# Optimization experiments

Hardware: AMD Instinct MI355X
Metric: run time of the kernel (lower is better)

The kernel has to match this reference:

```python
import jax, jax.numpy as jnp
import numpy as np

N, CS, CZ, CH, H, PQK, PV = 768, 384, 128, 16, 12, 4, 8
INF, EPS = 1e5, 1e-8


def setup_inputs() -> dict:
    key = jax.random.key(0)
    ks = jax.random.split(key, 12)
    w = lambda k, i, o: (jax.random.normal(k, (i, o), jnp.float32) * 0.02)
    inp = {
        's': jax.random.normal(ks[0], (N, CS), jnp.float32),
        'z': jax.random.normal(ks[1], (N, N, CZ), jnp.float32),
        'rot': jax.random.normal(ks[2], (N, 3, 3), jnp.float32),
        'trans': jax.random.normal(ks[3], (N, 3), jnp.float32),
        'mask': jnp.ones((N,), jnp.float32),
        'W_q': w(ks[4], CS, H * CH), 'b_q': jnp.zeros((H * CH,), jnp.float32),
        'W_kv': w(ks[5], CS, 2 * H * CH), 'b_kv': jnp.zeros((2 * H * CH,), jnp.float32),
        'W_qp': w(ks[6], CS, H * PQK * 3), 'b_qp': jnp.zeros((H * PQK * 3,), jnp.float32),
        'W_kvp': w(ks[7], CS, H * (PQK + PV) * 3), 'b_kvp': jnp.zeros((H * (PQK + PV) * 3,), jnp.float32),
        'W_b': w(ks[8], CZ, H), 'b_b': jnp.zeros((H,), jnp.float32),
        'head_weights': jnp.full((H,), 0.541324854612918, jnp.float32),  # softplus^-1(1)
        'W_out': w(ks[9], H * (CZ + CH + PV * 4), CS), 'b_out': jnp.zeros((CS,), jnp.float32),
    }
    return inp


def reference(s, z, rot, trans, mask, W_q, b_q, W_kv, b_kv, W_qp, b_qp, W_kvp, b_kvp,
              W_b, b_b, head_weights, W_out, b_out):
    n = s.shape[0]
    # scalar q/k/v
    q = (s @ W_q + b_q).reshape(n, H, CH)
    kv = (s @ W_kv + b_kv).reshape(n, H, 2 * CH)
    k, v = kv[..., :CH], kv[..., CH:]

    def make_points(W, b, P):
        p = (s @ W + b).reshape(n, 3, H * P)         # 3 contiguous coord chunks (x,y,z)
        p = jnp.transpose(p, (0, 2, 1))              # [n, H*P, 3]
        p = jnp.einsum('nij,npj->npi', rot, p) + trans[:, None, :]  # global frame
        return p.reshape(n, H, P, 3)

    q_pts = make_points(W_qp, b_qp, PQK)
    kv_pts = make_points(W_kvp, b_kvp, PQK + PV)
    k_pts, v_pts = kv_pts[:, :, :PQK], kv_pts[:, :, PQK:]

    b_pair = z @ W_b + b_b                                       # [n, n, H]
    a = jnp.einsum('qhc,khc->hqk', q, k) * np.sqrt(1.0 / (3 * CH))
    a = a + np.sqrt(1.0 / 3) * jnp.transpose(b_pair, (2, 0, 1))

    # point-distance attention term
    d2 = jnp.sum((q_pts[:, None] - k_pts[None]) ** 2, axis=-1)   # [q, k, H, Pqk]
    hw = jax.nn.softplus(head_weights) * np.sqrt(1.0 / (3 * (PQK * 9.0 / 2)))
    pt_att = -0.5 * jnp.sum(d2 * hw[None, None, :, None], axis=-1)  # [q, k, H]
    a = a + jnp.transpose(pt_att, (2, 0, 1))

    sq_mask = INF * (mask[:, None] * mask[None, :] - 1.0)
    a = jax.nn.softmax(a + sq_mask[None], axis=-1)               # [H, q, k]

    o = jnp.einsum('hqk,khc->qhc', a, v).reshape(n, H * CH)
    o_pt = jnp.einsum('hqk,khpc->qhpc', a, v_pts)                # [q, H, Pv, 3]
    o_pt = jnp.einsum('nba,nhpb->nhpa', rot, o_pt - trans[:, None, None, :])  # invert_apply
    o_pt_norm = jnp.sqrt(jnp.sum(o_pt ** 2, axis=-1) + EPS).reshape(n, H * PV)
    o_pt_flat = o_pt.reshape(n, H * PV, 3)
    o_pair = jnp.einsum('hqk,qkc->qhc', a, z).reshape(n, H * CZ)

    cat = jnp.concatenate([o, o_pt_flat[..., 0], o_pt_flat[..., 1], o_pt_flat[..., 2],
                           o_pt_norm, o_pair], axis=-1)          # [n, H*(CZ+CH+Pv*4)]
    return cat @ W_out + b_out
```

## Files before the change

### kernel.cpp

```cpp
#include <hip/hip_runtime.h>
#include <hip/hip_bf16.h>
#include <math.h>

#define NRES 768
#define CS   384
#define CZ   128
#define CH   16
#define NH   12
#define PQK  4
#define PV   8
#define QCOLS   (NH*CH)
#define KVCOLS  (2*NH*CH)
#define QPCOLS  (NH*PQK*3)
#define KVPCOLS (NH*(PQK+PV)*3)
#define CATC    (NH*(CZ+CH+PV*4))
#define NN      (NRES*NRES)

__global__ __launch_bounds__(256) void proj_kernel(
    const float* __restrict__ s,
    const float* __restrict__ Wq,  const float* __restrict__ bq,
    const float* __restrict__ Wkv, const float* __restrict__ bkv,
    const float* __restrict__ Wqp, const float* __restrict__ bqp,
    const float* __restrict__ Wkvp,const float* __restrict__ bkvp,
    float* __restrict__ proj_q, float* __restrict__ proj_kv,
    float* __restrict__ proj_qp, float* __restrict__ proj_kvp)
{
    __shared__ float Al[32][68];
    __shared__ float Bl[32][52];
    const int mt = blockIdx.x;
    const int gc0 = blockIdx.y * 48;
    const float* W; const float* bb; int ncol; float* dst; int c0;
    if (gc0 < 192)      { W=Wq;   bb=bq;   ncol=QCOLS;   dst=proj_q;   c0=gc0; }
    else if (gc0 < 576) { W=Wkv;  bb=bkv;  ncol=KVCOLS;  dst=proj_kv;  c0=gc0-192; }
    else if (gc0 < 720) { W=Wqp;  bb=bqp;  ncol=QPCOLS;  dst=proj_qp;  c0=gc0-576; }
    else                { W=Wkvp; bb=bkvp; ncol=KVPCOLS; dst=proj_kvp; c0=gc0-720; }
    const int tid = threadIdx.x;
    const int m0 = (tid & 15)*4;
    const int n0 = (tid >> 4)*3;
    float acc[4][3] = {};
    for (int kc = 0; kc < CS; kc += 32) {
        #pragma unroll
        for (int f = tid; f < 512; f += 256) {
            int r = f >> 3, c4 = (f & 7)*4;
            float4 v = *(const float4*)(s + (size_t)(mt*64+r)*CS + kc + c4);
            Al[c4][r]=v.x; Al[c4+1][r]=v.y; Al[c4+2][r]=v.z; Al[c4+3][r]=v.w;
        }
        for (int f = tid; f < 384; f += 256) {
            int r = f / 12, c4 = (f % 12)*4;
            *(float4*)&Bl[r][c4] = *(const float4*)(W + (size_t)(kc+r)*ncol + c0 + c4);
        }
        __syncthreads();
        #pragma unroll
        for (int kk = 0; kk < 32; ++kk) {
            float4 a = *(const float4*)&Al[kk][m0];
            float b0 = Bl[kk][n0], b1 = Bl[kk][n0+1], b2 = Bl[kk][n0+2];
            acc[0][0]+=a.x*b0; acc[0][1]+=a.x*b1; acc[0][2]+=a.x*b2;
            acc[1][0]+=a.y*b0; acc[1][1]+=a.y*b1; acc[1][2]+=a.y*b2;
            acc[2][0]+=a.z*b0; acc[2][1]+=a.z*b1; acc[2][2]+=a.z*b2;
            acc[3][0]+=a.w*b0; acc[3][1]+=a.w*b1; acc[3][2]+=a.w*b2;
        }
        __syncthreads();
    }
    #pragma unroll
    for (int r = 0; r < 4; ++r)
        #pragma unroll
        for (int c = 0; c < 3; ++c)
            dst[(size_t)(mt*64+m0+r)*ncol + c0+n0+c] = acc[r][c] + bb[c0+n0+c];
}

__global__ __launch_bounds__(256) void rotpts_kernel(
    const float* __restrict__ rot, const float* __restrict__ trans,
    const float* __restrict__ proj_q, const float* __restrict__ proj_kv,
    const float* __restrict__ proj_qp, const float* __restrict__ proj_kvp,
    const float* __restrict__ b_out,
    float* __restrict__ qfrag, float* __restrict__ kcat, float* __restrict__ vcatT,
    float* __restrict__ out)
{
    int g = blockIdx.x*256 + threadIdx.x;
    const int S0 = NRES*48;
    const int S1 = S0 + NRES*432;
    const int S2 = S1 + NRES*192;
    const int S3 = S2 + NRES*384;
    const int S4 = S3 + NRES*CS;
    if (g < S0) {
        int n = g/48, rem = g%48;
        int h = rem>>2, p = rem&3;
        float p0 = proj_qp[(size_t)n*QPCOLS + rem];
        float p1 = proj_qp[(size_t)n*QPCOLS + 48 + rem];
        float p2 = proj_qp[(size_t)n*QPCOLS + 96 + rem];
        const float* Rm = rot + (size_t)n*9; const float* t = trans + (size_t)n*3;
        float* dq = qfrag + ((size_t)n*12 + h)*28 + 16 + p*3;
        #pragma unroll
        for (int i = 0; i < 3; ++i)
            dq[i] = Rm[i*3]*p0 + Rm[i*3+1]*p1 + Rm[i*3+2]*p2 + t[i];
    } else if (g < S1) {
        int g2 = g - S0;
        int n = g2 % 768, t = g2 / 768;
        int h = t/36, u = t%36, p = u/3, i = u%3;
        int col = h*12 + p;
        float p0 = proj_kvp[(size_t)n*KVPCOLS + col];
        float p1 = proj_kvp[(size_t)n*KVPCOLS + 144 + col];
        float p2 = proj_kvp[(size_t)n*KVPCOLS + 288 + col];
        float val = rot[(size_t)n*9 + i*3]*p0 + rot[(size_t)n*9 + i*3+1]*p1
                  + rot[(size_t)n*9 + i*3+2]*p2 + trans[(size_t)n*3 + i];
        if (p < PQK) kcat[(size_t)(h*28 + 16 + p*3 + i)*NRES + n] = val;
        else         vcatT[(size_t)(h*40 + 16 + (p-4)*3 + i)*NRES + n] = val;
    } else if (g < S2) {
        int g3 = g - S1;
        int n = g3 / 192, c = g3 % 192;
        int h = c >> 4, cc = c & 15;
        qfrag[((size_t)n*12 + h)*28 + cc] = proj_q[(size_t)n*QCOLS + c];
    } else if (g < S3) {
        int g4 = g - S2;
        int n = g4 % 768, col = g4 / 768;
        int h = col >> 5, cc = col & 31;
        float val = proj_kv[(size_t)n*KVCOLS + col];
        if (cc < 16) kcat[(size_t)(h*28 + cc)*NRES + n] = val;
        else         vcatT[(size_t)(h*40 + (cc-16))*NRES + n] = val;
    } else if (g < S4) {
        int g5 = g - S3;
        out[g5] = b_out[g5 % CS];
    }
}

__global__ __launch_bounds__(256) void bias_kernel(
    const float* __restrict__ z, const float* __restrict__ mask,
    const float* __restrict__ W_b, const float* __restrict__ b_b,
    float* __restrict__ lg)
{
    int r = blockIdx.x*256 + threadIdx.x;
    int q = r / 768, k = r - q*768;
    const float4* zr = (const float4*)(z + (size_t)r*CZ);
    float acc[12] = {};
    #pragma unroll
    for (int c4 = 0; c4 < 32; ++c4) {
        float4 v = zr[c4];
        const float* w0 = W_b + c4*48;
        #pragma unroll
        for (int h = 0; h < 12; ++h)
            acc[h] += v.x*w0[h] + v.y*w0[12+h] + v.z*w0[24+h] + v.w*w0[36+h];
    }
    float mterm = 100000.0f*(mask[q]*mask[k] - 1.0f);
    const float scale_b = 0.5773502691896258f;
    #pragma unroll
    for (int h = 0; h < 12; ++h)
        lg[(size_t)h*NN + r] = scale_b*(acc[h] + b_b[h]) + mterm;
}

__global__ __launch_bounds__(256) void softmax_fused_kernel(
    float* __restrict__ lg, const float* __restrict__ qfrag, const float* __restrict__ kcat,
    const float* __restrict__ head_w, const float* __restrict__ vcatT,
    float* __restrict__ cat, float* __restrict__ optt)
{
    const int h = blockIdx.x % 12;
    const int q = (blockIdx.x / 12)*4 + (threadIdx.x >> 6);
    const int ln = threadIdx.x & 63;
    const float scale_qk = 0.14433756729740643f;
    float x = head_w[h];
    float sp = (x > 20.f) ? x : log1pf(__expf(x));
    float coef = -0.5f * sp * 0.13608276348795434f;

    float qf[28];
    const float* qp = qfrag + ((size_t)q*12 + h)*28;
    #pragma unroll
    for (int c = 0; c < 28; ++c) qf[c] = qp[c];

    float* arow = lg + (size_t)h*NN + (size_t)q*NRES;
    const float* kb = kcat + (size_t)h*28*NRES;
    float4 a[3];
    #pragma unroll
    for (int i = 0; i < 3; ++i) {
        a[i] = *(const float4*)(arow + ln*4 + i*256);
        float4 d = {0.f,0.f,0.f,0.f}, p2 = {0.f,0.f,0.f,0.f};
        #pragma unroll
        for (int c = 0; c < 16; ++c) {
            float4 kv = *(const float4*)(kb + (size_t)c*NRES + ln*4 + i*256);
            d.x += qf[c]*kv.x; d.y += qf[c]*kv.y; d.z += qf[c]*kv.z; d.w += qf[c]*kv.w;
        }
        #pragma unroll
        for (int c = 16; c < 28; ++c) {
            float4 kv = *(const float4*)(kb + (size_t)c*NRES + ln*4 + i*256);
            float t0 = qf[c]-kv.x, t1 = qf[c]-kv.y, t2 = qf[c]-kv.z, t3 = qf[c]-kv.w;
            p2.x += t0*t0; p2.y += t1*t1; p2.z += t2*t2; p2.w += t3*t3;
        }
        a[i].x += scale_qk*d.x + coef*p2.x;
        a[i].y += scale_qk*d.y + coef*p2.y;
        a[i].z += scale_qk*d.z + coef*p2.z;
        a[i].w += scale_qk*d.w + coef*p2.w;
    }
    float m = -1e30f;
    #pragma unroll
    for (int i=0;i<3;++i) m = fmaxf(m, fmaxf(fmaxf(a[i].x,a[i].y),fmaxf(a[i].z,a[i].w)));
    #pragma unroll
    for (int o=32;o>0;o>>=1) m = fmaxf(m, __shfl_xor(m,o,64));
    float ssum = 0.f;
    #pragma unroll
    for (int i=0;i<3;++i) {
        a[i].x = __expf(a[i].x-m); a[i].y = __expf(a[i].y-m);
        a[i].z = __expf(a[i].z-m); a[i].w = __expf(a[i].w-m);
        ssum += a[i].x + a[i].y + a[i].z + a[i].w;
    }
    #pragma unroll
    for (int o=32;o>0;o>>=1) ssum += __shfl_xor(ssum,o,64);
    float inv = 1.f/ssum;
    #pragma unroll
    for (int i=0;i<3;++i) {
        a[i].x*=inv; a[i].y*=inv; a[i].z*=inv; a[i].w*=inv;
        *(float4*)(arow + ln*4 + i*256) = a[i];
    }
    for (int col = 0; col < 40; ++col) {
        const float* vrow = vcatT + (size_t)(h*40+col)*NRES;
        float p = 0.f;
        #pragma unroll
        for (int i=0;i<3;++i) {
            float4 v = *(const float4*)(vrow + ln*4 + i*256);
            p += a[i].x*v.x + a[i].y*v.y + a[i].z*v.z + a[i].w*v.w;
        }
        #pragma unroll
        for (int o=32;o>0;o>>=1) p += __shfl_xor(p,o,64);
        if (ln == 0) {
            if (col < 16) cat[(size_t)q*CATC + h*16 + col] = p;
            else          optt[(size_t)q*288 + h*24 + (col-16)] = p;
        }
    }
}

__global__ __launch_bounds__(192) void opair_kernel(
    const float* __restrict__ z, const float* __restrict__ lg,
    const float* __restrict__ rot, const float* __restrict__ trans,
    const float* __restrict__ optt, float* __restrict__ cat)
{
    __shared__ float4 abuf4[2304];
    float* abuf = (float*)abuf4;
    const int q = blockIdx.x, tid = threadIdx.x;
    float* crow = cat + (size_t)q*CATC;

    for (int f = tid; f < 2304; f += 192) {
        int hh = f / 192, k4 = f % 192;
        abuf4[hh*192 + k4] = *(const float4*)(lg + (size_t)hh*NN + (size_t)q*NRES + k4*4);
    }
    __syncthreads();
    if (tid < 96) {
        int hh = tid>>3, p = tid&7;
        float b0 = optt[(size_t)q*288 + hh*24+p*3+0] - trans[q*3+0];
        float b1 = optt[(size_t)q*288 + hh*24+p*3+1] - trans[q*3+1];
        float b2 = optt[(size_t)q*288 + hh*24+p*3+2] - trans[q*3+2];
        const float* Rm = rot + (size_t)q*9;
        float v0 = Rm[0]*b0 + Rm[3]*b1 + Rm[6]*b2;
        float v1 = Rm[1]*b0 + Rm[4]*b1 + Rm[7]*b2;
        float v2 = Rm[2]*b0 + Rm[5]*b1 + Rm[8]*b2;
        crow[192 + tid] = v0;
        crow[288 + tid] = v1;
        crow[384 + tid] = v2;
        crow[480 + tid] = sqrtf(v0*v0 + v1*v1 + v2*v2 + 1e-8f);
    }
    const int h = tid >> 4, c8 = (tid & 15)*8;
    const float* zq = z + (size_t)q*NRES*CZ + c8;
    const float* ah = abuf + h*768;
    float4 acc0 = {0.f,0.f,0.f,0.f}, acc1 = {0.f,0.f,0.f,0.f};
    #pragma unroll 4
    for (int k = 0; k < NRES; ++k) {
        float aw = ah[k];
        float4 z0 = *(const float4*)(zq + (size_t)k*CZ);
        float4 z1 = *(const float4*)(zq + (size_t)k*CZ + 4);
        acc0.x += aw*z0.x; acc0.y += aw*z0.y; acc0.z += aw*z0.z; acc0.w += aw*z0.w;
        acc1.x += aw*z1.x; acc1.y += aw*z1.y; acc1.z += aw*z1.z; acc1.w += aw*z1.w;
    }
    *(float4*)(crow + 576 + h*128 + c8)     = acc0;
    *(float4*)(crow + 576 + h*128 + c8 + 4) = acc1;
}

__global__ __launch_bounds__(256) void outgemm_kernel(
    const float* __restrict__ cat, const float* __restrict__ W_out,
    float* __restrict__ out)
{
    __shared__ float Al[32][68];
    __shared__ float Bl[32][68];
    const int mt = blockIdx.x;
    const int nt = blockIdx.y;
    const int kt = blockIdx.z;
    const int tid = threadIdx.x;
    const int m0 = (tid & 15)*4, n0 = (tid >> 4)*4;
    float acc[4][4] = {};
    for (int ki = 0; ki < 11; ++ki) {
        int kc = kt*352 + ki*32;
        #pragma unroll
        for (int f = tid; f < 512; f += 256) {
            int r = f >> 3, c4 = (f & 7)*4;
            float4 v = *(const float4*)(cat + (size_t)(mt*64+r)*CATC + kc + c4);
            Al[c4][r]=v.x; Al[c4+1][r]=v.y; Al[c4+2][r]=v.z; Al[c4+3][r]=v.w;
        }
        #pragma unroll
        for (int f = tid; f < 512; f += 256) {
            int r = f >> 4, c4 = (f & 15)*4;
            *(float4*)&Bl[r][c4] = *(const float4*)(W_out + (size_t)(kc+r)*CS + nt*64 + c4);
        }
        __syncthreads();
        #pragma unroll
        for (int kk = 0; kk < 32; ++kk) {
            float4 a = *(const float4*)&Al[kk][m0];
            float4 b = *(const float4*)&Bl[kk][n0];
            acc[0][0]+=a.x*b.x; acc[0][1]+=a.x*b.y; acc[0][2]+=a.x*b.z; acc[0][3]+=a.x*b.w;
            acc[1][0]+=a.y*b.x; acc[1][1]+=a.y*b.y; acc[1][2]+=a.y*b.z; acc[1][3]+=a.y*b.w;
            acc[2][0]+=a.z*b.x; acc[2][1]+=a.z*b.y; acc[2][2]+=a.z*b.z; acc[2][3]+=a.z*b.w;
            acc[3][0]+=a.w*b.x; acc[3][1]+=a.w*b.y; acc[3][2]+=a.w*b.z; acc[3][3]+=a.w*b.w;
        }
        __syncthreads();
    }
    #pragma unroll
    for (int r = 0; r < 4; ++r)
        #pragma unroll
        for (int c = 0; c < 4; ++c)
            atomicAdd(&out[(size_t)(mt*64+m0+r)*CS + nt*64+n0+c], acc[r][c]);
}

extern "C" void kernel_launch(void* const* d_in, const int* in_sizes, int n_in,
                              void* d_out, int out_size, void* d_ws, size_t ws_size,
                              hipStream_t stream) {
    const float* s      = (const float*)d_in[0];
    const float* z      = (const float*)d_in[1];
    const float* rot    = (const float*)d_in[2];
    const float* trans  = (const float*)d_in[3];
    const float* mask   = (const float*)d_in[4];
    const float* W_q    = (const float*)d_in[5];
    const float* b_q    = (const float*)d_in[6];
    const float* W_kv   = (const float*)d_in[7];
    const float* b_kv   = (const float*)d_in[8];
    const float* W_qp   = (const float*)d_in[9];
    const float* b_qp   = (const float*)d_in[10];
    const float* W_kvp  = (const float*)d_in[11];
    const float* b_kvp  = (const float*)d_in[12];
    const float* W_b    = (const float*)d_in[13];
    const float* b_b    = (const float*)d_in[14];
    const float* head_w = (const float*)d_in[15];
    const float* W_out  = (const float*)d_in[16];
    const float* b_out  = (const float*)d_in[17];

    float* ws = (float*)d_ws;
    float* lg       = ws;
    float* proj_q   = ws;
    float* proj_kv  = ws + 147456;
    float* proj_qp  = ws + 442368;
    float* proj_kvp = ws + 552960;
    float* vcatT    = ws + 7077888;
    float* qfrag    = ws + 7446528;
    float* kcat     = ws + 7704576;
    float* optt     = ws + 7962624;
    float* cat      = ws + 8183808;
    float* out = (float*)d_out;

    proj_kernel<<<dim3(12,24), 256, 0, stream>>>(s, W_q, b_q, W_kv, b_kv, W_qp, b_qp, W_kvp, b_kvp,
                                                 proj_q, proj_kv, proj_qp, proj_kvp);
    rotpts_kernel<<<4320, 256, 0, stream>>>(rot, trans, proj_q, proj_kv, proj_qp, proj_kvp, b_out,
                                            qfrag, kcat, vcatT, out);
    bias_kernel<<<NN/256, 256, 0, stream>>>(z, mask, W_b, b_b, lg);
    softmax_fused_kernel<<<12*(NRES/4), 256, 0, stream>>>(lg, qfrag, kcat, head_w, vcatT, cat, optt);
    opair_kernel<<<NRES, 192, 0, stream>>>(z, lg, rot, trans, optt, cat);
    outgemm_kernel<<<dim3(12,6,6), 256, 0, stream>>>(cat, W_out, out);
}
```

Before: 800.9 us.

## Cache z as bf16 in bias pass and split opair over key halves

The bias kernel now also writes a bf16 copy of z. The opair kernel reads that copy instead of the fp32 z, which halves the bytes of the second full pass over z. Opair is split into two blocks per query, each covering half the keys, and the halves are combined with atomicAdd into a zero-initialised cat region; rotpts is extended to do that zeroing. The proj kernel now uses 32-row tiles for more blocks, and the softmax kernel runs 8 queries per 512-thread block. The cost is an extra bf16 write pass, reduced precision in o_pair, and atomics.

```diff
diff --git a/kernel.cpp b/kernel.cpp
--- a/kernel.cpp
+++ b/kernel.cpp
@@ -16,6 +16,16 @@
 #define CATC    (NH*(CZ+CH+PV*4))
 #define NN      (NRES*NRES)
 
+static __device__ __forceinline__ unsigned pack_bf16(float a, float b) {
+    unsigned ua = __float_as_uint(a);
+    unsigned ub = __float_as_uint(b);
+    ua = (ua + 0x7fffu + ((ua >> 16) & 1u)) >> 16;
+    ub = (ub + 0x7fffu + ((ub >> 16) & 1u)) & 0xffff0000u;
+    return ua | ub;
+}
+#define BFLO(u) __uint_as_float((u) << 16)
+#define BFHI(u) __uint_as_float((u) & 0xffff0000u)
+
 __global__ __launch_bounds__(256) void proj_kernel(
     const float* __restrict__ s,
     const float* __restrict__ Wq,  const float* __restrict__ bq,
@@ -25,7 +35,7 @@
     float* __restrict__ proj_q, float* __restrict__ proj_kv,
     float* __restrict__ proj_qp, float* __restrict__ proj_kvp)
 {
-    __shared__ float Al[32][68];
+    __shared__ float Al[32][36];
     __shared__ float Bl[32][52];
     const int mt = blockIdx.x;
     const int gc0 = blockIdx.y * 48;
@@ -35,14 +45,13 @@
     else if (gc0 < 720) { W=Wqp;  bb=bqp;  ncol=QPCOLS;  dst=proj_qp;  c0=gc0-576; }
     else                { W=Wkvp; bb=bkvp; ncol=KVPCOLS; dst=proj_kvp; c0=gc0-720; }
     const int tid = threadIdx.x;
-    const int m0 = (tid & 15)*4;
+    const int m0 = (tid & 15)*2;
     const int n0 = (tid >> 4)*3;
-    float acc[4][3] = {};
+    float acc[2][3] = {};
     for (int kc = 0; kc < CS; kc += 32) {
-        #pragma unroll
-        for (int f = tid; f < 512; f += 256) {
-            int r = f >> 3, c4 = (f & 7)*4;
-            float4 v = *(const float4*)(s + (size_t)(mt*64+r)*CS + kc + c4);
+        {
+            int r = tid >> 3, c4 = (tid & 7)*4;
+            float4 v = *(const float4*)(s + (size_t)(mt*32+r)*CS + kc + c4);
             Al[c4][r]=v.x; Al[c4+1][r]=v.y; Al[c4+2][r]=v.z; Al[c4+3][r]=v.w;
         }
         for (int f = tid; f < 384; f += 256) {
@@ -52,20 +61,18 @@
         __syncthreads();
         #pragma unroll
         for (int kk = 0; kk < 32; ++kk) {
-            float4 a = *(const float4*)&Al[kk][m0];
+            float2 a = *(const float2*)&Al[kk][m0];
             float b0 = Bl[kk][n0], b1 = Bl[kk][n0+1], b2 = Bl[kk][n0+2];
             acc[0][0]+=a.x*b0; acc[0][1]+=a.x*b1; acc[0][2]+=a.x*b2;
             acc[1][0]+=a.y*b0; acc[1][1]+=a.y*b1; acc[1][2]+=a.y*b2;
-            acc[2][0]+=a.z*b0; acc[2][1]+=a.z*b1; acc[2][2]+=a.z*b2;
-            acc[3][0]+=a.w*b0; acc[3][1]+=a.w*b1; acc[3][2]+=a.w*b2;
         }
         __syncthreads();
     }
     #pragma unroll
-    for (int r = 0; r < 4; ++r)
+    for (int r = 0; r < 2; ++r)
         #pragma unroll
         for (int c = 0; c < 3; ++c)
-            dst[(size_t)(mt*64+m0+r)*ncol + c0+n0+c] = acc[r][c] + bb[c0+n0+c];
+            dst[(size_t)(mt*32+m0+r)*ncol + c0+n0+c] = acc[r][c] + bb[c0+n0+c];
 }
 
 __global__ __launch_bounds__(256) void rotpts_kernel(
@@ -74,7 +81,7 @@
     const float* __restrict__ proj_qp, const float* __restrict__ proj_kvp,
     const float* __restrict__ b_out,
     float* __restrict__ qfrag, float* __restrict__ kcat, float* __restrict__ vcatT,
-    float* __restrict__ out)
+    float* __restrict__ out, float* __restrict__ cat)
 {
     int g = blockIdx.x*256 + threadIdx.x;
     const int S0 = NRES*48;
@@ -82,6 +89,7 @@
     const int S2 = S1 + NRES*192;
     const int S3 = S2 + NRES*384;
     const int S4 = S3 + NRES*CS;
+    const int S5 = S4 + NRES*1536;
     if (g < S0) {
         int n = g/48, rem = g%48;
         int h = rem>>2, p = rem&3;
@@ -120,17 +128,22 @@
     } else if (g < S4) {
         int g5 = g - S3;
         out[g5] = b_out[g5 % CS];
+    } else if (g < S5) {
+        int g6 = g - S4;
+        int q = g6 / 1536, c = g6 % 1536;
+        cat[(size_t)q*CATC + 576 + c] = 0.f;
     }
 }
 
 __global__ __launch_bounds__(256) void bias_kernel(
     const float* __restrict__ z, const float* __restrict__ mask,
     const float* __restrict__ W_b, const float* __restrict__ b_b,
-    float* __restrict__ lg)
+    float* __restrict__ lg, unsigned short* __restrict__ zh)
 {
     int r = blockIdx.x*256 + threadIdx.x;
     int q = r / 768, k = r - q*768;
     const float4* zr = (const float4*)(z + (size_t)r*CZ);
+    unsigned* zhr = (unsigned*)(zh + (size_t)r*CZ);
     float acc[12] = {};
     #pragma unroll
     for (int c4 = 0; c4 < 32; ++c4) {
@@ -139,6 +152,8 @@
         #pragma unroll
         for (int h = 0; h < 12; ++h)
             acc[h] += v.x*w0[h] + v.y*w0[12+h] + v.z*w0[24+h] + v.w*w0[36+h];
+        uint2 u; u.x = pack_bf16(v.x, v.y); u.y = pack_bf16(v.z, v.w);
+        *(uint2*)(zhr + c4*2) = u;
     }
     float mterm = 100000.0f*(mask[q]*mask[k] - 1.0f);
     const float scale_b = 0.5773502691896258f;
@@ -147,13 +162,13 @@
         lg[(size_t)h*NN + r] = scale_b*(acc[h] + b_b[h]) + mterm;
 }
 
-__global__ __launch_bounds__(256) void softmax_fused_kernel(
+__global__ __launch_bounds__(512) void softmax_fused_kernel(
     float* __restrict__ lg, const float* __restrict__ qfrag, const float* __restrict__ kcat,
     const float* __restrict__ head_w, const float* __restrict__ vcatT,
     float* __restrict__ cat, float* __restrict__ optt)
 {
     const int h = blockIdx.x % 12;
-    const int q = (blockIdx.x / 12)*4 + (threadIdx.x >> 6);
+    const int q = (blockIdx.x / 12)*8 + (threadIdx.x >> 6);
     const int ln = threadIdx.x & 63;
     const float scale_qk = 0.14433756729740643f;
     float x = head_w[h];
@@ -226,21 +241,21 @@
 }
 
 __global__ __launch_bounds__(192) void opair_kernel(
-    const float* __restrict__ z, const float* __restrict__ lg,
+    const unsigned short* __restrict__ zh, const float* __restrict__ lg,
     const float* __restrict__ rot, const float* __restrict__ trans,
     const float* __restrict__ optt, float* __restrict__ cat)
 {
-    __shared__ float4 abuf4[2304];
-    float* abuf = (float*)abuf4;
-    const int q = blockIdx.x, tid = threadIdx.x;
+    __shared__ float abuf[12*385];
+    const int q = blockIdx.x >> 1, half = blockIdx.x & 1;
+    const int tid = threadIdx.x;
     float* crow = cat + (size_t)q*CATC;
 
-    for (int f = tid; f < 2304; f += 192) {
-        int hh = f / 192, k4 = f % 192;
-        abuf4[hh*192 + k4] = *(const float4*)(lg + (size_t)hh*NN + (size_t)q*NRES + k4*4);
+    for (int f = tid; f < 4608; f += 192) {
+        int hh = f / 384, k = f % 384;
+        abuf[hh*385 + k] = lg[(size_t)hh*NN + (size_t)q*NRES + half*384 + k];
     }
     __syncthreads();
-    if (tid < 96) {
+    if (half == 0 && tid < 96) {
         int hh = tid>>3, p = tid&7;
         float b0 = optt[(size_t)q*288 + hh*24+p*3+0] - trans[q*3+0];
         float b1 = optt[(size_t)q*288 + hh*24+p*3+1] - trans[q*3+1];
@@ -255,19 +270,23 @@
         crow[480 + tid] = sqrtf(v0*v0 + v1*v1 + v2*v2 + 1e-8f);
     }
     const int h = tid >> 4, c8 = (tid & 15)*8;
-    const float* zq = z + (size_t)q*NRES*CZ + c8;
-    const float* ah = abuf + h*768;
-    float4 acc0 = {0.f,0.f,0.f,0.f}, acc1 = {0.f,0.f,0.f,0.f};
+    const unsigned* zq = (const unsigned*)zh + ((size_t)(q*768 + half*384))*64 + (tid & 15)*4;
+    const float* ah = abuf + h*385;
+    float a0=0,a1=0,a2=0,a3=0,a4=0,a5=0,a6=0,a7=0;
     #pragma unroll 4
-    for (int k = 0; k < NRES; ++k) {
+    for (int k = 0; k < 384; ++k) {
         float aw = ah[k];
-        float4 z0 = *(const float4*)(zq + (size_t)k*CZ);
-        float4 z1 = *(const float4*)(zq + (size_t)k*CZ + 4);
-        acc0.x += aw*z0.x; acc0.y += aw*z0.y; acc0.z += aw*z0.z; acc0.w += aw*z0.w;
-        acc1.x += aw*z1.x; acc1.y += aw*z1.y; acc1.z += aw*z1.z; acc1.w += aw*z1.w;
-    }
-    *(float4*)(crow + 576 + h*128 + c8)     = acc0;
-    *(float4*)(crow + 576 + h*128 + c8 + 4) = acc1;
+        uint4 zv = *(const uint4*)(zq + (size_t)k*64);
+        a0 += aw*BFLO(zv.x); a1 += aw*BFHI(zv.x);
+        a2 += aw*BFLO(zv.y); a3 += aw*BFHI(zv.y);
+        a4 += aw*BFLO(zv.z); a5 += aw*BFHI(zv.z);
+        a6 += aw*BFLO(zv.w); a7 += aw*BFHI(zv.w);
+    }
+    float* dst = crow + 576 + h*128 + c8;
+    atomicAdd(dst+0, a0); atomicAdd(dst+1, a1);
+    atomicAdd(dst+2, a2); atomicAdd(dst+3, a3);
+    atomicAdd(dst+4, a4); atomicAdd(dst+5, a5);
+    atomicAdd(dst+6, a6); atomicAdd(dst+7, a7);
 }
 
 __global__ __launch_bounds__(256) void outgemm_kernel(
@@ -347,14 +366,15 @@
     float* kcat     = ws + 7704576;
     float* optt     = ws + 7962624;
     float* cat      = ws + 8183808;
+    unsigned short* zh = (unsigned short*)(ws + 9805824);
     float* out = (float*)d_out;
 
-    proj_kernel<<<dim3(12,24), 256, 0, stream>>>(s, W_q, b_q, W_kv, b_kv, W_qp, b_qp, W_kvp, b_kvp,
+    proj_kernel<<<dim3(24,24), 256, 0, stream>>>(s, W_q, b_q, W_kv, b_kv, W_qp, b_qp, W_kvp, b_kvp,
                                                  proj_q, proj_kv, proj_qp, proj_kvp);
-    rotpts_kernel<<<4320, 256, 0, stream>>>(rot, trans, proj_q, proj_kv, proj_qp, proj_kvp, b_out,
-                                            qfrag, kcat, vcatT, out);
-    bias_kernel<<<NN/256, 256, 0, stream>>>(z, mask, W_b, b_b, lg);
-    softmax_fused_kernel<<<12*(NRES/4), 256, 0, stream>>>(lg, qfrag, kcat, head_w, vcatT, cat, optt);
-    opair_kernel<<<NRES, 192, 0, stream>>>(z, lg, rot, trans, optt, cat);
+    rotpts_kernel<<<8928, 256, 0, stream>>>(rot, trans, proj_q, proj_kv, proj_qp, proj_kvp, b_out,
+                                            qfrag, kcat, vcatT, out, cat);
+    bias_kernel<<<NN/256, 256, 0, stream>>>(z, mask, W_b, b_b, lg, zh);
+    softmax_fused_kernel<<<12*(NRES/8), 512, 0, stream>>>(lg, qfrag, kcat, head_w, vcatT, cat, optt);
+    opair_kernel<<<NRES*2, 192, 0, stream>>>(zh, lg, rot, trans, optt, cat);
     outgemm_kernel<<<dim3(12,6,6), 256, 0, stream>>>(cat, W_out, out);
 }
```

New measurement: 930.3 us. 16.2% more time.
